# Kernel tuning notes

Measured on AMD Instinct MI355X. Metric: run time of the kernel, lower is better.

Reference implementation:

```python
import jax, jax.numpy as jnp
import numpy as np

# Module config (init_kwargs) and input dims
N, H, W, C = 8, 256, 256, 32
OH, OW = 512, 512  # size = (OH, OW); square so the original's H/W-swap quirks are benign


def setup_inputs() -> dict:
    key = jax.random.key(0)
    img = jax.random.normal(key, (N, H, W, C), dtype=jnp.float32)
    return {"img": img}


def reference(img):
    # Replicates BilinearInterpolate.build + call for square in/out sizes.
    _, H_, W_, _ = img.shape
    y_scale = H_ / OH
    x_scale = W_ / OW

    # Source sampling coordinates (half-pixel-center convention, clamped at 0)
    gy = jnp.maximum((jnp.arange(OH, dtype=jnp.float32) + 0.5) * y_scale - 0.5, 0.0)[:, None]  # (OH,1)
    gx = jnp.maximum((jnp.arange(OW, dtype=jnp.float32) + 0.5) * x_scale - 0.5, 0.0)[None, :]  # (1,OW)

    y0 = jnp.floor(gy).astype(jnp.int32)  # (OH,1)
    x0 = jnp.floor(gx).astype(jnp.int32)  # (1,OW)
    # Original guards the y-increment with W-1 and the x-increment with H-1 (swapped);
    # with H == W this is identical to the correct bounds.
    y1 = y0 + (y0 < W_ - 1).astype(jnp.int32)
    x1 = x0 + (x0 < H_ - 1).astype(jnp.int32)

    # Four-corner gather; advanced indexing broadcasts (OH,1)x(1,OW) -> (OH,OW),
    # result per corner is (N, OH, OW, C).
    v00 = img[:, y0, x0, :]
    v01 = img[:, y0, x1, :]  # +x
    v10 = img[:, y1, x0, :]  # +y
    v11 = img[:, y1, x1, :]

    # Fractional weights: h0 = y frac, w0 = x frac (matches l[...,0]/l[...,1])
    h0 = (gy - y0.astype(jnp.float32))[None, :, :, None]  # (1,OH,1,1)
    w0 = (gx - x0.astype(jnp.float32))[None, :, :, None]  # (1,1,OW,1)
    h1 = 1.0 - h0
    w1 = 1.0 - w0

    return h1 * (w1 * v00 + w0 * v01) + h0 * (w1 * v10 + w0 * v11)
```

## Files before the change

kernel.cpp:

```cpp
#include <hip/hip_runtime.h>


#define IH 256
#define IW 256
#define OHW 512
#define C4 8
#define NBLK 32768u

typedef float f4 __attribute__((ext_vector_type(4)));

__global__ __launch_bounds__(256) void bilinear2x_kernel(
    const float* __restrict__ img, float* __restrict__ out) {
    unsigned b  = blockIdx.x;
    unsigned wb = (b & 7u) * (NBLK / 8u) + (b >> 3);
    unsigned tid = wb * 256u + threadIdx.x;

    unsigned c4 = tid & (C4 - 1);
    unsigned ox = (tid >> 3) & (OHW - 1);
    unsigned j  = (tid >> 12) & (IH - 1);
    unsigned n  = tid >> 20;

    float gx = fmaxf(0.5f * (float)ox - 0.25f, 0.0f);
    int x0 = (int)gx;
    float w0 = gx - (float)x0;
    int x1 = x0 + (x0 < IW - 1);
    float w1 = 1.0f - w0;

    int rA = (int)j - 1; rA = rA < 0 ? 0 : rA;
    int rB = (int)j;
    int rC = (int)j + 1; rC = rC > IH - 1 ? IH - 1 : rC;

    const f4* base = (const f4*)img;
    size_t nb = (size_t)n * (IH * IW * C4);
    const f4* pA = base + nb + (size_t)rA * (IW * C4);
    const f4* pB = base + nb + (size_t)rB * (IW * C4);
    const f4* pC = base + nb + (size_t)rC * (IW * C4);
    size_t o0 = (size_t)x0 * C4 + c4;
    size_t o1 = (size_t)x1 * C4 + c4;

    f4 a0 = pA[o0], a1 = pA[o1];
    f4 b0 = pB[o0], b1 = pB[o1];
    f4 c0 = pC[o0], c1 = pC[o1];

    f4 ra = w1 * a0 + w0 * a1;
    f4 rb = w1 * b0 + w0 * b1;
    f4 rc = w1 * c0 + w0 * c1;

    f4 re = 0.25f * ra + 0.75f * rb;
    f4 ro = 0.75f * rb + 0.25f * rc;

    f4* ob = (f4*)out;
    size_t oe = (((size_t)n * OHW + 2 * j) * OHW + ox) * C4 + c4;
    __builtin_nontemporal_store(re, ob + oe);
    __builtin_nontemporal_store(ro, ob + oe + (size_t)OHW * C4);
}

extern "C" void kernel_launch(void* const* d_in, const int* in_sizes, int n_in,
                              void* d_out, int out_size, void* d_ws, size_t ws_size,
                              hipStream_t stream) {
    const float* img = (const float*)d_in[0];
    float* out = (float*)d_out;
    dim3 grid(NBLK);
    dim3 block(256);
    bilinear2x_kernel<<<grid, block, 0, stream>>>(img, out);
}
```

Before: 328.6 us.

## Stream 16 rows per thread reusing horizontally interpolated rows

Each thread now handles a strip of 16 input rows for one output column and channel group. It carries the x-interpolated previous rows in registers, so each input row is loaded and blended once instead of three times. The grid shrinks to 2048 blocks with a launch-bounds occupancy hint. Nontemporal stores are replaced by ordinary stores, which may change cache behaviour on the large output write, and each thread exposes less independent memory work.

```diff
diff --git a/kernel.cpp b/kernel.cpp
--- a/kernel.cpp
+++ b/kernel.cpp
@@ -5,20 +5,21 @@
 #define IW 256
 #define OHW 512
 #define C4 8
-#define NBLK 32768u
+#define JPER 16
 
 typedef float f4 __attribute__((ext_vector_type(4)));
 
-__global__ __launch_bounds__(256) void bilinear2x_kernel(
+__global__ __launch_bounds__(256, 8) void bilinear2x_kernel(
     const float* __restrict__ img, float* __restrict__ out) {
-    unsigned b  = blockIdx.x;
-    unsigned wb = (b & 7u) * (NBLK / 8u) + (b >> 3);
-    unsigned tid = wb * 256u + threadIdx.x;
+    unsigned bx  = blockIdx.x;
+    unsigned oxc = bx & 15u;
+    unsigned jc  = (bx >> 4) & 15u;
+    unsigned n   = bx >> 8;
 
-    unsigned c4 = tid & (C4 - 1);
-    unsigned ox = (tid >> 3) & (OHW - 1);
-    unsigned j  = (tid >> 12) & (IH - 1);
-    unsigned n  = tid >> 20;
+    unsigned c4  = threadIdx.x & (C4 - 1);
+    unsigned oxl = threadIdx.x >> 3;
+    unsigned ox  = oxc * 32u + oxl;
+    int j0 = (int)(jc * JPER);
 
     float gx = fmaxf(0.5f * (float)ox - 0.25f, 0.0f);
     int x0 = (int)gx;
@@ -26,33 +27,38 @@
     int x1 = x0 + (x0 < IW - 1);
     float w1 = 1.0f - w0;
 
-    int rA = (int)j - 1; rA = rA < 0 ? 0 : rA;
-    int rB = (int)j;
-    int rC = (int)j + 1; rC = rC > IH - 1 ? IH - 1 : rC;
-
-    const f4* base = (const f4*)img;
-    size_t nb = (size_t)n * (IH * IW * C4);
-    const f4* pA = base + nb + (size_t)rA * (IW * C4);
-    const f4* pB = base + nb + (size_t)rB * (IW * C4);
-    const f4* pC = base + nb + (size_t)rC * (IW * C4);
+    const f4* base = (const f4*)img + (size_t)n * (IH * IW * C4);
     size_t o0 = (size_t)x0 * C4 + c4;
     size_t o1 = (size_t)x1 * C4 + c4;
 
+    int rA = j0 - 1; if (rA < 0) rA = 0;
+    const f4* pA = base + (size_t)rA * (IW * C4);
+    const f4* pB = base + (size_t)j0 * (IW * C4);
     f4 a0 = pA[o0], a1 = pA[o1];
     f4 b0 = pB[o0], b1 = pB[o1];
-    f4 c0 = pC[o0], c1 = pC[o1];
-
-    f4 ra = w1 * a0 + w0 * a1;
-    f4 rb = w1 * b0 + w0 * b1;
-    f4 rc = w1 * c0 + w0 * c1;
-
-    f4 re = 0.25f * ra + 0.75f * rb;
-    f4 ro = 0.75f * rb + 0.25f * rc;
+    f4 xa = w1 * a0 + w0 * a1;
+    f4 xb = w1 * b0 + w0 * b1;
 
     f4* ob = (f4*)out;
-    size_t oe = (((size_t)n * OHW + 2 * j) * OHW + ox) * C4 + c4;
-    __builtin_nontemporal_store(re, ob + oe);
-    __builtin_nontemporal_store(ro, ob + oe + (size_t)OHW * C4);
+    size_t oe = (((size_t)n * OHW + 2 * (size_t)j0) * OHW + ox) * C4 + c4;
+    const size_t rowstep = (size_t)OHW * C4;
+
+#pragma unroll 4
+    for (int t = 0; t < JPER; ++t) {
+        int j = j0 + t;
+        int rC = j + 1; if (rC > IH - 1) rC = IH - 1;
+        const f4* pC = base + (size_t)rC * (IW * C4);
+        f4 cc0 = pC[o0], cc1 = pC[o1];
+        f4 xc = w1 * cc0 + w0 * cc1;
+
+        f4 re = 0.25f * xa + 0.75f * xb;
+        f4 ro = 0.75f * xb + 0.25f * xc;
+        ob[oe] = re;
+        ob[oe + rowstep] = ro;
+        oe += 2 * rowstep;
+
+        xa = xb; xb = xc;
+    }
 }
 
 extern "C" void kernel_launch(void* const* d_in, const int* in_sizes, int n_in,
@@ -60,7 +66,7 @@
                               hipStream_t stream) {
     const float* img = (const float*)d_in[0];
     float* out = (float*)d_out;
-    dim3 grid(NBLK);
+    dim3 grid(2048);
     dim3 block(256);
     bilinear2x_kernel<<<grid, block, 0, stream>>>(img, out);
 }
```

New measurement: 320.1 us. 1.03x faster.
